# Kernel optimization log

Hardware: AMD Instinct MI355X
Metric: run time of the kernel (lower is better)

Reference implementation:

```python
import jax, jax.numpy as jnp
import numpy as np

B, N, D, K = 1024, 36, 256, 8  # batch, num_features(fixed 36 by docstring), embed_size, text_K


def setup_inputs() -> dict:
    key = jax.random.key(0)
    ks = jax.random.split(key, 5)
    texts = jax.random.normal(ks[0], (B, N, D), dtype=jnp.float32)
    # Xavier-uniform-style init matching module.init_weights()
    r_k = np.sqrt(6.0) / np.sqrt(D + D)
    r_v = np.sqrt(6.0) / np.sqrt(D + K)
    r_u = np.sqrt(6.0) / np.sqrt(K + 1)
    W = jax.random.uniform(ks[1], (K, D, D), minval=-r_k, maxval=r_k, dtype=jnp.float32)
    Wb = jnp.zeros((K, D), dtype=jnp.float32)
    V1w = jax.random.uniform(ks[2], (K, D), minval=-r_v, maxval=r_v, dtype=jnp.float32)
    V1b = jnp.zeros((K,), dtype=jnp.float32)
    V2w = jax.random.uniform(ks[3], (K, D), minval=-r_v, maxval=r_v, dtype=jnp.float32)
    V2b = jnp.zeros((K,), dtype=jnp.float32)
    Uw = jax.random.uniform(ks[4], (K,), minval=-r_u, maxval=r_u, dtype=jnp.float32)
    Ub = jnp.zeros((), dtype=jnp.float32)
    return {"texts": texts, "W": W, "Wb": Wb, "V1w": V1w, "V1b": V1b,
            "V2w": V2w, "V2b": V2b, "Uw": Uw, "Ub": Ub}


def reference(texts, W, Wb, V1w, V1b, V2w, V2b, Uw, Ub):
    # bilinear term: (W_k x_n + b_k) . x_m  -> [B,K,N,N]
    Wx = jnp.einsum('kcd,bnd->bknc', W, texts) + Wb[None, :, None, :]
    first = jnp.einsum('bknc,bmc->bknm', Wx, texts)
    # outer-sum term: V1.x_n + V2.x_m (per k)
    v1 = jnp.einsum('kd,bnd->bkn', V1w, texts) + V1b[None, :, None]  # [B,K,N]
    v2 = jnp.einsum('kd,bmd->bkm', V2w, texts) + V2b[None, :, None]  # [B,K,N]
    T = jnp.tanh(first + v1[..., None] + v2[:, :, None, :])  # [B,K,N,N]
    # faithful to torch: flatten [K,N,N] contiguously then view as (N*N, K)
    flat = T.reshape(T.shape[0], N * N, K)
    logits = (flat @ Uw + Ub).reshape(T.shape[0], N, N)
    return jax.nn.softmax(logits, axis=-1)
```

## Files before the change

kernel.cpp:

```cpp
#include <hip/hip_runtime.h>
#include <math.h>

#define NB 1024
#define NF 36
#define ED 256
#define NK 8
#define NN2 1296
#define QPK 162

typedef _Float16 f16;
typedef f16 f16x4 __attribute__((ext_vector_type(4)));
typedef f16 f16x8 __attribute__((ext_vector_type(8)));
typedef float f32x4 __attribute__((ext_vector_type(4)));

#define WXSTR 136
#define WXHSZ 13056
#define NFRAG 1536

#define XH_OFF  0
#define WXH_OFF 24576
#define V_OFF   (24576 + WXHSZ)
#define SMEM_MAIN (V_OFF + (72 + 72 + 9 + 324) * 4)

#define PVH_OFF 0
#define PVL_OFF 8192
#define PP_OFF  16384
#define SMEM_PREP 28672

#define TWO_LOG2E 2.8853900817779268f
#define C1F (0.0625f * TWO_LOG2E)

__device__ __forceinline__ f32x4 mfma16(f16x8 a, f16x8 b, f32x4 c) {
    return __builtin_amdgcn_mfma_f32_16x16x32_f16(a, b, c, 0, 0, 0);
}

__global__ __launch_bounds__(256, 4) void prep_all(
    const float* __restrict__ W, f16x8* __restrict__ WfH,
    const float* __restrict__ texts, f16x8* __restrict__ XfH,
    const float* __restrict__ V1w, const float* __restrict__ V1b,
    const float* __restrict__ V2w, const float* __restrict__ V2b,
    const float* __restrict__ Wb, float* __restrict__ v12)
{
    extern __shared__ char psmem[];
    const int blk = blockIdx.x;
    const int t = threadIdx.x;
    const int wave = t >> 6, lane = t & 63;

    if (blk < 128) {
        const int k = blk >> 4, ct = blk & 15;
        f16* Wl = (f16*)psmem;
        {
            const int r = t >> 4, seg = t & 15;
            const float* src = W + ((size_t)(k * 256 + ct * 16 + r)) * 256 + seg * 16;
            f16* d = Wl + r * 264 + seg * 16;
            #pragma unroll
            for (int j4 = 0; j4 < 4; ++j4) {
                float4 a = ((const float4*)src)[j4];
                d[j4 * 4 + 0] = (f16)(a.x * 16.0f);
                d[j4 * 4 + 1] = (f16)(a.y * 16.0f);
                d[j4 * 4 + 2] = (f16)(a.z * 16.0f);
                d[j4 * 4 + 3] = (f16)(a.w * 16.0f);
            }
        }
        __syncthreads();
        f16x8* dst = WfH + (size_t)(k * 16 + ct) * 8 * 64;
        #pragma unroll
        for (int e0 = 0; e0 < 2; ++e0) {
            const int e = t + e0 * 256;
            const int kc = e >> 6, el = e & 63, qd = el >> 4, l15 = el & 15;
            dst[e] = *(const f16x8*)(Wl + l15 * 264 + (kc * 4 + qd) * 8);
        }
        return;
    }

    f16x8* VfH = (f16x8*)(psmem + PVH_OFF);
    f16x8* VfL = (f16x8*)(psmem + PVL_OFF);
    f32x4* Pp  = (f32x4*)(psmem + PP_OFF);

    const int b = blk - 128;
    const float* xb = texts + (size_t)b * NF * ED;

    #pragma unroll
    for (int i0 = 0; i0 < 2; ++i0) {
        int i = t + i0 * 256;
        int kc = (i >> 6) & 7, ln = i & 63;
        int q = ln >> 4, col = ln & 15;
        int which = col >> 3, kk = col & 7;
        const float* src  = (which ? V2w : V1w) + kk * 256 + kc * 32 + q * 8;
        const float* srcb = Wb + kk * 256 + kc * 32 + q * 8;
        f16x8 hi, lo;
        #pragma unroll
        for (int j = 0; j < 8; ++j) {
            float sv = src[j] + (which ? srcb[j] : 0.f);
            sv *= 16.0f;
            f16 h = (f16)sv;
            hi[j] = h;
            lo[j] = (f16)(sv - (float)h);
        }
        VfH[i] = hi;
        VfL[i] = lo;
    }

    f16x8 FH[6], FL[6];
    #pragma unroll
    for (int i0 = 0; i0 < 6; ++i0) {
        int i = t + i0 * 256;
        int rt = i >> 9, kc = (i >> 6) & 7;
        int q = lane >> 4, l15 = lane & 15;
        int row = rt * 16 + l15;
        f16x8 hi, lo;
        if (row < NF) {
            const float* s = xb + row * ED + kc * 32 + q * 8;
            float4 a = *(const float4*)s;
            float4 c = *(const float4*)(s + 4);
            float v[8] = {a.x, a.y, a.z, a.w, c.x, c.y, c.z, c.w};
            #pragma unroll
            for (int j = 0; j < 8; ++j) {
                f16 h = (f16)v[j];
                hi[j] = h;
                lo[j] = (f16)(v[j] - (float)h);
            }
        } else {
            #pragma unroll
            for (int j = 0; j < 8; ++j) { hi[j] = (f16)0.f; lo[j] = (f16)0.f; }
        }
        FH[i0] = hi;
        FL[i0] = lo;
        XfH[(size_t)b * NFRAG + i] = hi;
    }
    __syncthreads();

    f32x4 pacc[3];
    #pragma unroll
    for (int rt = 0; rt < 3; ++rt) pacc[rt] = (f32x4){0.f, 0.f, 0.f, 0.f};
    #pragma unroll
    for (int rt = 0; rt < 3; ++rt) {
        #pragma unroll
        for (int s = 0; s < 2; ++s) {
            const int i0 = rt * 2 + s;
            const int kc = wave + 4 * s;
            f16x8 bh = VfH[kc * 64 + lane];
            f16x8 bl = VfL[kc * 64 + lane];
            pacc[rt] = mfma16(FH[i0], bh, pacc[rt]);
            pacc[rt] = mfma16(FH[i0], bl, pacc[rt]);
            pacc[rt] = mfma16(FL[i0], bh, pacc[rt]);
        }
    }
    #pragma unroll
    for (int rt = 0; rt < 3; ++rt)
        Pp[(wave * 3 + rt) * 64 + lane] = pacc[rt];
    __syncthreads();

    if (wave < 3) {
        f32x4 acc = Pp[(0 * 3 + wave) * 64 + lane];
        #pragma unroll
        for (int w = 1; w < 4; ++w) acc += Pp[(w * 3 + wave) * 64 + lane];
        const int q = lane >> 4, l15 = lane & 15;
        const int which = l15 >> 3, kk = l15 & 7;
        const float bias = which ? V2b[kk] : V1b[kk];
        #pragma unroll
        for (int r = 0; r < 4; ++r) {
            const int n = wave * 16 + q * 4 + r;
            if (n < NF)
                v12[((size_t)b * 16 + l15) * NF + n] = acc[r] * 0.0625f + bias;
        }
    }
}

#define P1_STEP(ACC, WKP, H, KC) do {                                         \
    f16x8 w0_ = (WKP)[((((H) * 8 + wave) * 8) + (KC)) * 64 + lane];           \
    f16x8 w1_ = (WKP)[((((H) * 8 + wave + 4) * 8) + (KC)) * 64 + lane];       \
    _Pragma("unroll")                                                         \
    for (int rt_ = 0; rt_ < 3; ++rt_) {                                       \
        f16x8 ah_ = Xh[(rt_ * 8 + (KC)) * 64 + lane];                         \
        ACC[rt_][0] = mfma16(w0_, ah_, ACC[rt_][0]);                          \
        ACC[rt_][1] = mfma16(w1_, ah_, ACC[rt_][1]);                          \
    }                                                                         \
} while (0)

#define P2_TILE(IT, H, KK) do {                                               \
    const int p_ = wave + (IT) * 4;                                           \
    if (p_ < 9) {                                                             \
        const int nt_ = p_ / 3, mt_ = p_ % 3;                                 \
        const f16* wp_ = Wxh + (nt_ * 16 + l15) * WXSTR + quad * 8;           \
        _Pragma("unroll")                                                     \
        for (int kc2_ = 0; kc2_ < 4; ++kc2_) {                                \
            f16x8 pah_ = *(const f16x8*)(wp_ + kc2_ * 32);                    \
            f16x8 pbh_ = Xh[(mt_ * 8 + (H) * 4 + kc2_) * 64 + lane];          \
            sacc[KK][IT] = mfma16(pah_, pbh_, sacc[KK][IT]);                  \
        }                                                                     \
    }                                                                         \
} while (0)

#define ZERO_ACC(ACC) do {                                                    \
    _Pragma("unroll")                                                         \
    for (int i_ = 0; i_ < 3; ++i_) {                                          \
        ACC[i_][0] = (f32x4){0.f, 0.f, 0.f, 0.f};                             \
        ACC[i_][1] = (f32x4){0.f, 0.f, 0.f, 0.f};                             \
    }                                                                         \
} while (0)

#define STORE_WX(ACC) do {                                                    \
    _Pragma("unroll")                                                         \
    for (int rt_ = 0; rt_ < 3; ++rt_) {                                       \
        const int n_ = rt_ * 16 + l15;                                        \
        _Pragma("unroll")                                                     \
        for (int j2_ = 0; j2_ < 2; ++j2_) {                                   \
            const int cb_ = (j2_ ? (wave + 4) : wave) * 16 + quad * 4;        \
            f16x4 h4_;                                                        \
            _Pragma("unroll")                                                 \
            for (int r_ = 0; r_ < 4; ++r_) h4_[r_] = (f16)(ACC[rt_][j2_][r_]);\
            *(f16x4*)(Wxh + n_ * WXSTR + cb_) = h4_;                          \
        }                                                                     \
    }                                                                         \
} while (0)

#define SEG_FUSED(ACC, WKP, H1, HP, KKP) do {                                 \
    _Pragma("unroll")                                                         \
    for (int kc_ = 0; kc_ < 8; ++kc_) {                                       \
        P1_STEP(ACC, WKP, H1, kc_);                                           \
        if (kc_ == 1) P2_TILE(0, HP, KKP);                                    \
        if (kc_ == 3) P2_TILE(1, HP, KKP);                                    \
        if (kc_ == 5) P2_TILE(2, HP, KKP);                                    \
    }                                                                         \
} while (0)

__global__ __launch_bounds__(256, 4) void ntn_main(
    const f16x8* __restrict__ XfHG,
    const f16x8* __restrict__ WfH,
    const float* __restrict__ v12,
    const float* __restrict__ Uw, const float* __restrict__ Ubp,
    float* __restrict__ out)
{
    extern __shared__ char smem[];
    f16x8* Xh   = (f16x8*)(smem + XH_OFF);
    f16*   Wxh  = (f16*)(smem + WXH_OFF);
    float* v1s2 = (float*)(smem + V_OFF);
    float* v2s2 = v1s2 + 72;
    float* Uws  = v1s2 + 144;
    float* Ls   = v1s2 + 153;

    const int id  = blockIdx.x;
    const int xcd = id & 7;
    const int rem = id >> 3;
    const int kp  = rem & 3;
    const int b   = ((rem >> 2) << 3) | xcd;
    const int k0  = kp * 2;

    const int t    = threadIdx.x;
    const int wave = t >> 6;
    const int lane = t & 63;
    const int quad = lane >> 4;
    const int l15  = lane & 15;

    {
        const f16x8* gh = XfHG + (size_t)b * NFRAG;
        #pragma unroll
        for (int i = 0; i < 6; ++i) Xh[t + i * 256] = gh[t + i * 256];
    }
    if (t < 144) {
        const int r = t / 36, n = t - r * 36;
        const int which = r & 1, kq = r >> 1;
        float v = v12[((size_t)b * 16 + which * 8 + (k0 + kq)) * NF + n] * TWO_LOG2E;
        (which ? v2s2 : v1s2)[kq * 36 + n] = v;
    }
    if (t < 8) Uws[t] = Uw[t];
    if (t == 8) Uws[8] = Ubp[0];
    __syncthreads();

    const f16x8* Wk0 = WfH + (size_t)k0 * 8192;
    const f16x8* Wk1 = Wk0 + 8192;

    f32x4 sacc[2][3];
    #pragma unroll
    for (int kk = 0; kk < 2; ++kk)
        #pragma unroll
        for (int it = 0; it < 3; ++it) sacc[kk][it] = (f32x4){0.f, 0.f, 0.f, 0.f};

    f32x4 acc[3][2];

    ZERO_ACC(acc);
    #pragma unroll
    for (int kc = 0; kc < 8; ++kc) P1_STEP(acc, Wk0, 0, kc);
    STORE_WX(acc);
    __syncthreads();

    ZERO_ACC(acc);
    SEG_FUSED(acc, Wk1, 0, 0, 0);
    __syncthreads();
    STORE_WX(acc);
    __syncthreads();

    ZERO_ACC(acc);
    SEG_FUSED(acc, Wk0, 1, 0, 1);
    __syncthreads();
    STORE_WX(acc);
    __syncthreads();

    ZERO_ACC(acc);
    SEG_FUSED(acc, Wk1, 1, 1, 0);
    __syncthreads();
    STORE_WX(acc);
    __syncthreads();

    P2_TILE(0, 1, 1);
    P2_TILE(1, 1, 1);
    P2_TILE(2, 1, 1);

    __syncthreads();
    float* Ts = (float*)Wxh;
    #pragma unroll
    for (int kk = 0; kk < 2; ++kk)
        #pragma unroll
        for (int it = 0; it < 3; ++it) {
            const int p = wave + it * 4;
            if (p < 9) {
                const int nt = p / 3, mt = p % 3;
                const int m = mt * 16 + l15;
                if (m < NF) {
                    #pragma unroll
                    for (int r = 0; r < 4; ++r) {
                        const int n = nt * 16 + quad * 4 + r;
                        if (n < NF) {
                            float x = sacc[kk][it][r] * C1F
                                      + v1s2[kk * 36 + n] + v2s2[kk * 36 + m];
                            float e = exp2f(x);
                            const int idx = kk * NN2 + n * NF + m;
                            Ts[idx + (idx >> 3)] = 1.f - 2.f / (e + 1.f);
                        }
                    }
                }
            }
        }
    __syncthreads();
    #pragma unroll
    for (int u0 = 0; u0 < 2; ++u0) {
        const int u = t + u0 * 256;
        if (u < 324) {
            const float* tp = Ts + u * 9;
            float lg = Uws[8];
            #pragma unroll
            for (int j = 0; j < 8; ++j) lg += Uws[j] * tp[j];
            Ls[u] = lg;
        }
    }
    __syncthreads();
    #pragma unroll
    for (int rr0 = 0; rr0 < 3; ++rr0) {
        const int rr = wave + rr0 * 4;
        if (rr < 9) {
            float v = (lane < NF) ? Ls[rr * 36 + lane] : -INFINITY;
            float mx = v;
            #pragma unroll
            for (int off = 32; off > 0; off >>= 1) mx = fmaxf(mx, __shfl_xor(mx, off));
            float e = (lane < NF) ? __expf(v - mx) : 0.f;
            float sm = e;
            #pragma unroll
            for (int off = 32; off > 0; off >>= 1) sm += __shfl_xor(sm, off);
            if (lane < NF)
                out[(size_t)b * NN2 + kp * 324 + rr * 36 + lane] = e / sm;
        }
    }
}

extern "C" void kernel_launch(void* const* d_in, const int* in_sizes, int n_in,
                              void* d_out, int out_size, void* d_ws, size_t ws_size,
                              hipStream_t stream) {
    const float* texts = (const float*)d_in[0];
    const float* W     = (const float*)d_in[1];
    const float* Wb    = (const float*)d_in[2];
    const float* V1w   = (const float*)d_in[3];
    const float* V1b   = (const float*)d_in[4];
    const float* V2w   = (const float*)d_in[5];
    const float* V2b   = (const float*)d_in[6];
    const float* Uw    = (const float*)d_in[7];
    const float* Ub    = (const float*)d_in[8];

    char* ws = (char*)d_ws;
    f16x8* WfH = (f16x8*)ws;
    f16x8* XfH = (f16x8*)(ws + (1 << 20));
    float* v12 = (float*)(ws + (1 << 20) + (size_t)NB * NFRAG * 16);
    float* outp = (float*)d_out;

    hipFuncSetAttribute((const void*)prep_all,
                        hipFuncAttributeMaxDynamicSharedMemorySize, SMEM_PREP);
    hipFuncSetAttribute((const void*)ntn_main,
                        hipFuncAttributeMaxDynamicSharedMemorySize, SMEM_MAIN);

    prep_all<<<128 + NB, 256, SMEM_PREP, stream>>>(W, WfH, texts, XfH,
                                                   V1w, V1b, V2w, V2b, Wb, v12);
    ntn_main<<<NB * NK / 2, 256, SMEM_MAIN, stream>>>(XfH, WfH, v12, Uw, Ub, outp);
}
```

Baseline: 182.0 us.

## Process both K slices per phase with compacted padded X tile in LDS

Restructures the main kernel so each phase computes Wx for both k slices at once, sharing each X fragment load across four MFMAs and halving the number of phase/barrier rounds. The padded third row tile of X is compacted into a small LDS region, with a shared zero buffer serving the padding rows, and Wx rows beyond 36 are neither stored nor read. LDS is reorganized into two Wx buffers. This doubles accumulator registers (acc becomes 3x2x2), which may pressure occupancy at the 4-blocks launch bound.

```diff
diff --git a/kernel.cpp b/kernel.cpp
--- a/kernel.cpp
+++ b/kernel.cpp
@@ -6,7 +6,6 @@
 #define ED 256
 #define NK 8
 #define NN2 1296
-#define QPK 162
 
 typedef _Float16 f16;
 typedef f16 f16x4 __attribute__((ext_vector_type(4)));
@@ -14,12 +13,13 @@
 typedef float f32x4 __attribute__((ext_vector_type(4)));
 
 #define WXSTR 136
-#define WXHSZ 13056
 #define NFRAG 1536
 
-#define XH_OFF  0
-#define WXH_OFF 24576
-#define V_OFF   (24576 + WXHSZ)
+#define XC2_OFF 16384
+#define ZB_OFF  18432
+#define WX0_OFF 18448
+#define WX1_OFF (WX0_OFF + 9792)
+#define V_OFF   (WX1_OFF + 9792)
 #define SMEM_MAIN (V_OFF + (72 + 72 + 9 + 324) * 4)
 
 #define PVH_OFF 0
@@ -32,6 +32,15 @@
 
 __device__ __forceinline__ f32x4 mfma16(f16x8 a, f16x8 b, f32x4 c) {
     return __builtin_amdgcn_mfma_f32_16x16x32_f16(a, b, c, 0, 0, 0);
+}
+
+__device__ __forceinline__ const f16x8* xfragp(const char* smem, int f, int lane) {
+    const int l15 = lane & 15, q = (lane >> 4) & 3;
+    int off;
+    if (f < 16) off = (f * 64 + lane) * 16;
+    else        off = (l15 < 4) ? (XC2_OFF + (((f - 16) * 16) + q * 4 + l15) * 16)
+                                : ZB_OFF;
+    return (const f16x8*)(smem + off);
 }
 
 __global__ __launch_bounds__(256, 4) void prep_all(
@@ -167,61 +176,68 @@
     }
 }
 
-#define P1_STEP(ACC, WKP, H, KC) do {                                         \
-    f16x8 w0_ = (WKP)[((((H) * 8 + wave) * 8) + (KC)) * 64 + lane];           \
-    f16x8 w1_ = (WKP)[((((H) * 8 + wave + 4) * 8) + (KC)) * 64 + lane];       \
+#define P1S(ACC, H, KC) do {                                                  \
+    f16x8 w00_ = Wk0[((((H) * 8 + wave) * 8) + (KC)) * 64 + lane];            \
+    f16x8 w01_ = Wk0[((((H) * 8 + wave + 4) * 8) + (KC)) * 64 + lane];        \
+    f16x8 w10_ = Wk1[((((H) * 8 + wave) * 8) + (KC)) * 64 + lane];            \
+    f16x8 w11_ = Wk1[((((H) * 8 + wave + 4) * 8) + (KC)) * 64 + lane];        \
     _Pragma("unroll")                                                         \
     for (int rt_ = 0; rt_ < 3; ++rt_) {                                       \
-        f16x8 ah_ = Xh[(rt_ * 8 + (KC)) * 64 + lane];                         \
-        ACC[rt_][0] = mfma16(w0_, ah_, ACC[rt_][0]);                          \
-        ACC[rt_][1] = mfma16(w1_, ah_, ACC[rt_][1]);                          \
+        f16x8 ah_ = *xfragp(smem, rt_ * 8 + (KC), lane);                      \
+        ACC[rt_][0][0] = mfma16(w00_, ah_, ACC[rt_][0][0]);                   \
+        ACC[rt_][1][0] = mfma16(w01_, ah_, ACC[rt_][1][0]);                   \
+        ACC[rt_][0][1] = mfma16(w10_, ah_, ACC[rt_][0][1]);                   \
+        ACC[rt_][1][1] = mfma16(w11_, ah_, ACC[rt_][1][1]);                   \
     }                                                                         \
 } while (0)
 
-#define P2_TILE(IT, H, KK) do {                                               \
+#define P2_TILE2(IT, H) do {                                                  \
     const int p_ = wave + (IT) * 4;                                           \
     if (p_ < 9) {                                                             \
         const int nt_ = p_ / 3, mt_ = p_ % 3;                                 \
-        const f16* wp_ = Wxh + (nt_ * 16 + l15) * WXSTR + quad * 8;           \
+        const int row_ = nt_ * 16 + l15;                                      \
+        const int cr_ = row_ > 35 ? 35 : row_;    \
+        const f16* w0p_ = Wxh0 + cr_ * WXSTR + quad * 8;                      \
+        const f16* w1p_ = Wxh1 + cr_ * WXSTR + quad * 8;                      \
         _Pragma("unroll")                                                     \
         for (int kc2_ = 0; kc2_ < 4; ++kc2_) {                                \
-            f16x8 pah_ = *(const f16x8*)(wp_ + kc2_ * 32);                    \
-            f16x8 pbh_ = Xh[(mt_ * 8 + (H) * 4 + kc2_) * 64 + lane];          \
-            sacc[KK][IT] = mfma16(pah_, pbh_, sacc[KK][IT]);                  \
+            f16x8 xb_ = *xfragp(smem, mt_ * 8 + (H) * 4 + kc2_, lane);        \
+            f16x8 a0_ = *(const f16x8*)(w0p_ + kc2_ * 32);                    \
+            f16x8 a1_ = *(const f16x8*)(w1p_ + kc2_ * 32);                    \
+            sacc[0][IT] = mfma16(a0_, xb_, sacc[0][IT]);                      \
+            sacc[1][IT] = mfma16(a1_, xb_, sacc[1][IT]);                      \
         }                                                                     \
     }                                                                         \
 } while (0)
 
 #define ZERO_ACC(ACC) do {                                                    \
     _Pragma("unroll")                                                         \
-    for (int i_ = 0; i_ < 3; ++i_) {                                          \
-        ACC[i_][0] = (f32x4){0.f, 0.f, 0.f, 0.f};                             \
-        ACC[i_][1] = (f32x4){0.f, 0.f, 0.f, 0.f};                             \
-    }                                                                         \
+    for (int i_ = 0; i_ < 3; ++i_)                                            \
+        _Pragma("unroll")                                                     \
+        for (int j_ = 0; j_ < 2; ++j_) {                                      \
+            ACC[i_][j_][0] = (f32x4){0.f, 0.f, 0.f, 0.f};                     \
+            ACC[i_][j_][1] = (f32x4){0.f, 0.f, 0.f, 0.f};                     \
+        }                                                                     \
 } while (0)
 
-#define STORE_WX(ACC) do {                                                    \
+#define STORE_WX2(ACC) do {                                                   \
     _Pragma("unroll")                                                         \
     for (int rt_ = 0; rt_ < 3; ++rt_) {                                       \
         const int n_ = rt_ * 16 + l15;                                        \
-        _Pragma("unroll")                                                     \
-        for (int j2_ = 0; j2_ < 2; ++j2_) {                                   \
-            const int cb_ = (j2_ ? (wave + 4) : wave) * 16 + quad * 4;        \
-            f16x4 h4_;                                                        \
+        if (rt_ < 2 || l15 < 4) {                                             \
             _Pragma("unroll")                                                 \
-            for (int r_ = 0; r_ < 4; ++r_) h4_[r_] = (f16)(ACC[rt_][j2_][r_]);\
-            *(f16x4*)(Wxh + n_ * WXSTR + cb_) = h4_;                          \
+            for (int j2_ = 0; j2_ < 2; ++j2_) {                               \
+                const int cb_ = (j2_ ? (wave + 4) : wave) * 16 + quad * 4;    \
+                f16x4 h0_, h1_;                                               \
+                _Pragma("unroll")                                             \
+                for (int r_ = 0; r_ < 4; ++r_) {                              \
+                    h0_[r_] = (f16)(ACC[rt_][j2_][0][r_]);                    \
+                    h1_[r_] = (f16)(ACC[rt_][j2_][1][r_]);                    \
+                }                                                             \
+                *(f16x4*)(Wxh0 + n_ * WXSTR + cb_) = h0_;                     \
+                *(f16x4*)(Wxh1 + n_ * WXSTR + cb_) = h1_;                     \
+            }                                                                 \
         }                                                                     \
-    }                                                                         \
-} while (0)
-
-#define SEG_FUSED(ACC, WKP, H1, HP, KKP) do {                                 \
-    _Pragma("unroll")                                                         \
-    for (int kc_ = 0; kc_ < 8; ++kc_) {                                       \
-        P1_STEP(ACC, WKP, H1, kc_);                                           \
-        if (kc_ == 1) P2_TILE(0, HP, KKP);                                    \
-        if (kc_ == 3) P2_TILE(1, HP, KKP);                                    \
-        if (kc_ == 5) P2_TILE(2, HP, KKP);                                    \
     }                                                                         \
 } while (0)
 
@@ -233,8 +249,8 @@
     float* __restrict__ out)
 {
     extern __shared__ char smem[];
-    f16x8* Xh   = (f16x8*)(smem + XH_OFF);
-    f16*   Wxh  = (f16*)(smem + WXH_OFF);
+    f16*   Wxh0 = (f16*)(smem + WX0_OFF);
+    f16*   Wxh1 = (f16*)(smem + WX1_OFF);
     float* v1s2 = (float*)(smem + V_OFF);
     float* v2s2 = v1s2 + 72;
     float* Uws  = v1s2 + 144;
@@ -256,7 +272,22 @@
     {
         const f16x8* gh = XfHG + (size_t)b * NFRAG;
         #pragma unroll
-        for (int i = 0; i < 6; ++i) Xh[t + i * 256] = gh[t + i * 256];
+        for (int i0 = 0; i0 < 4; ++i0)
+            *(f16x8*)(smem + (size_t)(t + i0 * 256) * 16) = gh[t + i0 * 256];
+        #pragma unroll
+        for (int i0 = 4; i0 < 6; ++i0) {
+            const int e = t + i0 * 256;
+            f16x8 v = gh[e];
+            const int kc = (e >> 6) - 16;
+            if (l15 < 4)
+                *(f16x8*)(smem + XC2_OFF + (size_t)(kc * 16 + quad * 4 + l15) * 16) = v;
+        }
+        if (t == 0) {
+            f16x8 z;
+            #pragma unroll
+            for (int j = 0; j < 8; ++j) z[j] = (f16)0.f;
+            *(f16x8*)(smem + ZB_OFF) = z;
+        }
     }
     if (t < 144) {
         const int r = t / 36, n = t - r * 36;
@@ -277,38 +308,32 @@
         #pragma unroll
         for (int it = 0; it < 3; ++it) sacc[kk][it] = (f32x4){0.f, 0.f, 0.f, 0.f};
 
-    f32x4 acc[3][2];
+    f32x4 acc[3][2][2];
 
     ZERO_ACC(acc);
     #pragma unroll
-    for (int kc = 0; kc < 8; ++kc) P1_STEP(acc, Wk0, 0, kc);
-    STORE_WX(acc);
+    for (int kc = 0; kc < 8; ++kc) P1S(acc, 0, kc);
+    STORE_WX2(acc);
     __syncthreads();
 
     ZERO_ACC(acc);
-    SEG_FUSED(acc, Wk1, 0, 0, 0);
-    __syncthreads();
-    STORE_WX(acc);
-    __syncthreads();
-
-    ZERO_ACC(acc);
-    SEG_FUSED(acc, Wk0, 1, 0, 1);
-    __syncthreads();
-    STORE_WX(acc);
-    __syncthreads();
-
-    ZERO_ACC(acc);
-    SEG_FUSED(acc, Wk1, 1, 1, 0);
-    __syncthreads();
-    STORE_WX(acc);
-    __syncthreads();
-
-    P2_TILE(0, 1, 1);
-    P2_TILE(1, 1, 1);
-    P2_TILE(2, 1, 1);
-
-    __syncthreads();
-    float* Ts = (float*)Wxh;
+    #pragma unroll
+    for (int kc = 0; kc < 8; ++kc) {
+        P1S(acc, 1, kc);
+        if (kc == 1) P2_TILE2(0, 0);
+        if (kc == 3) P2_TILE2(1, 0);
+        if (kc == 5) P2_TILE2(2, 0);
+    }
+    __syncthreads();
+    STORE_WX2(acc);
+    __syncthreads();
+
+    P2_TILE2(0, 1);
+    P2_TILE2(1, 1);
+    P2_TILE2(2, 1);
+
+    __syncthreads();
+    float* Ts = (float*)Wxh0;
     #pragma unroll
     for (int kk = 0; kk < 2; ++kk)
         #pragma unroll
```

Measured after the change: 190.5 us. +4.7%, slower.

## Fuse per-batch text conversion and V projection into main kernel

Applied to the files above, without the earlier changes.

Moves the fp32-to-fp16 hi/lo conversion of texts and the V1/V2 projection out of the prep kernel and into ntn_main. Each main block now reads raw texts, builds its X fragments in LDS, and computes the v1/v2 terms itself, reusing the Wx LDS area as reduction scratch. This drops the XfH and v12 workspace round trip and shrinks the prep kernel to W packing only. In exchange, the per-batch conversion and projection MFMAs are repeated in each of the four blocks per batch, and an extra barrier is added before the first Wx store.

```diff
diff --git a/kernel.cpp b/kernel.cpp
--- a/kernel.cpp
+++ b/kernel.cpp
@@ -6,7 +6,6 @@
 #define ED 256
 #define NK 8
 #define NN2 1296
-#define QPK 162
 
 typedef _Float16 f16;
 typedef f16 f16x4 __attribute__((ext_vector_type(4)));
@@ -22,10 +21,7 @@
 #define V_OFF   (24576 + WXHSZ)
 #define SMEM_MAIN (V_OFF + (72 + 72 + 9 + 324) * 4)
 
-#define PVH_OFF 0
-#define PVL_OFF 8192
-#define PP_OFF  16384
-#define SMEM_PREP 28672
+#define SMEM_PREP 8448
 
 #define TWO_LOG2E 2.8853900817779268f
 #define C1F (0.0625f * TWO_LOG2E)
@@ -34,136 +30,34 @@
     return __builtin_amdgcn_mfma_f32_16x16x32_f16(a, b, c, 0, 0, 0);
 }
 
-__global__ __launch_bounds__(256, 4) void prep_all(
-    const float* __restrict__ W, f16x8* __restrict__ WfH,
-    const float* __restrict__ texts, f16x8* __restrict__ XfH,
-    const float* __restrict__ V1w, const float* __restrict__ V1b,
-    const float* __restrict__ V2w, const float* __restrict__ V2b,
-    const float* __restrict__ Wb, float* __restrict__ v12)
+__global__ __launch_bounds__(256, 4) void wpack(
+    const float* __restrict__ W, f16x8* __restrict__ WfH)
 {
     extern __shared__ char psmem[];
     const int blk = blockIdx.x;
     const int t = threadIdx.x;
-    const int wave = t >> 6, lane = t & 63;
-
-    if (blk < 128) {
-        const int k = blk >> 4, ct = blk & 15;
-        f16* Wl = (f16*)psmem;
-        {
-            const int r = t >> 4, seg = t & 15;
-            const float* src = W + ((size_t)(k * 256 + ct * 16 + r)) * 256 + seg * 16;
-            f16* d = Wl + r * 264 + seg * 16;
-            #pragma unroll
-            for (int j4 = 0; j4 < 4; ++j4) {
-                float4 a = ((const float4*)src)[j4];
-                d[j4 * 4 + 0] = (f16)(a.x * 16.0f);
-                d[j4 * 4 + 1] = (f16)(a.y * 16.0f);
-                d[j4 * 4 + 2] = (f16)(a.z * 16.0f);
-                d[j4 * 4 + 3] = (f16)(a.w * 16.0f);
-            }
-        }
-        __syncthreads();
-        f16x8* dst = WfH + (size_t)(k * 16 + ct) * 8 * 64;
-        #pragma unroll
-        for (int e0 = 0; e0 < 2; ++e0) {
-            const int e = t + e0 * 256;
-            const int kc = e >> 6, el = e & 63, qd = el >> 4, l15 = el & 15;
-            dst[e] = *(const f16x8*)(Wl + l15 * 264 + (kc * 4 + qd) * 8);
-        }
-        return;
-    }
-
-    f16x8* VfH = (f16x8*)(psmem + PVH_OFF);
-    f16x8* VfL = (f16x8*)(psmem + PVL_OFF);
-    f32x4* Pp  = (f32x4*)(psmem + PP_OFF);
-
-    const int b = blk - 128;
-    const float* xb = texts + (size_t)b * NF * ED;
-
-    #pragma unroll
-    for (int i0 = 0; i0 < 2; ++i0) {
-        int i = t + i0 * 256;
-        int kc = (i >> 6) & 7, ln = i & 63;
-        int q = ln >> 4, col = ln & 15;
-        int which = col >> 3, kk = col & 7;
-        const float* src  = (which ? V2w : V1w) + kk * 256 + kc * 32 + q * 8;
-        const float* srcb = Wb + kk * 256 + kc * 32 + q * 8;
-        f16x8 hi, lo;
-        #pragma unroll
-        for (int j = 0; j < 8; ++j) {
-            float sv = src[j] + (which ? srcb[j] : 0.f);
-            sv *= 16.0f;
-            f16 h = (f16)sv;
-            hi[j] = h;
-            lo[j] = (f16)(sv - (float)h);
-        }
-        VfH[i] = hi;
-        VfL[i] = lo;
-    }
-
-    f16x8 FH[6], FL[6];
-    #pragma unroll
-    for (int i0 = 0; i0 < 6; ++i0) {
-        int i = t + i0 * 256;
-        int rt = i >> 9, kc = (i >> 6) & 7;
-        int q = lane >> 4, l15 = lane & 15;
-        int row = rt * 16 + l15;
-        f16x8 hi, lo;
-        if (row < NF) {
-            const float* s = xb + row * ED + kc * 32 + q * 8;
-            float4 a = *(const float4*)s;
-            float4 c = *(const float4*)(s + 4);
-            float v[8] = {a.x, a.y, a.z, a.w, c.x, c.y, c.z, c.w};
-            #pragma unroll
-            for (int j = 0; j < 8; ++j) {
-                f16 h = (f16)v[j];
-                hi[j] = h;
-                lo[j] = (f16)(v[j] - (float)h);
-            }
-        } else {
-            #pragma unroll
-            for (int j = 0; j < 8; ++j) { hi[j] = (f16)0.f; lo[j] = (f16)0.f; }
-        }
-        FH[i0] = hi;
-        FL[i0] = lo;
-        XfH[(size_t)b * NFRAG + i] = hi;
-    }
-    __syncthreads();
-
-    f32x4 pacc[3];
-    #pragma unroll
-    for (int rt = 0; rt < 3; ++rt) pacc[rt] = (f32x4){0.f, 0.f, 0.f, 0.f};
-    #pragma unroll
-    for (int rt = 0; rt < 3; ++rt) {
-        #pragma unroll
-        for (int s = 0; s < 2; ++s) {
-            const int i0 = rt * 2 + s;
-            const int kc = wave + 4 * s;
-            f16x8 bh = VfH[kc * 64 + lane];
-            f16x8 bl = VfL[kc * 64 + lane];
-            pacc[rt] = mfma16(FH[i0], bh, pacc[rt]);
-            pacc[rt] = mfma16(FH[i0], bl, pacc[rt]);
-            pacc[rt] = mfma16(FL[i0], bh, pacc[rt]);
-        }
-    }
-    #pragma unroll
-    for (int rt = 0; rt < 3; ++rt)
-        Pp[(wave * 3 + rt) * 64 + lane] = pacc[rt];
-    __syncthreads();
-
-    if (wave < 3) {
-        f32x4 acc = Pp[(0 * 3 + wave) * 64 + lane];
-        #pragma unroll
-        for (int w = 1; w < 4; ++w) acc += Pp[(w * 3 + wave) * 64 + lane];
-        const int q = lane >> 4, l15 = lane & 15;
-        const int which = l15 >> 3, kk = l15 & 7;
-        const float bias = which ? V2b[kk] : V1b[kk];
-        #pragma unroll
-        for (int r = 0; r < 4; ++r) {
-            const int n = wave * 16 + q * 4 + r;
-            if (n < NF)
-                v12[((size_t)b * 16 + l15) * NF + n] = acc[r] * 0.0625f + bias;
-        }
+    const int k = blk >> 4, ct = blk & 15;
+    f16* Wl = (f16*)psmem;
+    {
+        const int r = t >> 4, seg = t & 15;
+        const float* src = W + ((size_t)(k * 256 + ct * 16 + r)) * 256 + seg * 16;
+        f16* d = Wl + r * 264 + seg * 16;
+        #pragma unroll
+        for (int j4 = 0; j4 < 4; ++j4) {
+            float4 a = ((const float4*)src)[j4];
+            d[j4 * 4 + 0] = (f16)(a.x * 16.0f);
+            d[j4 * 4 + 1] = (f16)(a.y * 16.0f);
+            d[j4 * 4 + 2] = (f16)(a.z * 16.0f);
+            d[j4 * 4 + 3] = (f16)(a.w * 16.0f);
+        }
+    }
+    __syncthreads();
+    f16x8* dst = WfH + (size_t)(k * 16 + ct) * 8 * 64;
+    #pragma unroll
+    for (int e0 = 0; e0 < 2; ++e0) {
+        const int e = t + e0 * 256;
+        const int kc = e >> 6, el = e & 63, qd = el >> 4, l15 = el & 15;
+        dst[e] = *(const f16x8*)(Wl + l15 * 264 + (kc * 4 + qd) * 8);
     }
 }
 
@@ -226,9 +120,11 @@
 } while (0)
 
 __global__ __launch_bounds__(256, 4) void ntn_main(
-    const f16x8* __restrict__ XfHG,
+    const float* __restrict__ texts,
     const f16x8* __restrict__ WfH,
-    const float* __restrict__ v12,
+    const float* __restrict__ V1w, const float* __restrict__ V1b,
+    const float* __restrict__ V2w, const float* __restrict__ V2b,
+    const float* __restrict__ Wb,
     const float* __restrict__ Uw, const float* __restrict__ Ubp,
     float* __restrict__ out)
 {
@@ -253,21 +149,90 @@
     const int quad = lane >> 4;
     const int l15  = lane & 15;
 
+    const float* xb = texts + (size_t)b * NF * ED;
+    f16x8 FH[6], FL[6];
+    #pragma unroll
+    for (int i0 = 0; i0 < 6; ++i0) {
+        const int i = t + i0 * 256;
+        const int rt = i >> 9, kc = (i >> 6) & 7;
+        const int row = rt * 16 + l15;
+        f16x8 hi, lo;
+        if (row < NF) {
+            const float* s = xb + row * ED + kc * 32 + quad * 8;
+            float4 a = *(const float4*)s;
+            float4 c = *(const float4*)(s + 4);
+            float v[8] = {a.x, a.y, a.z, a.w, c.x, c.y, c.z, c.w};
+            #pragma unroll
+            for (int j = 0; j < 8; ++j) {
+                f16 h = (f16)v[j];
+                hi[j] = h;
+                lo[j] = (f16)(v[j] - (float)h);
+            }
+        } else {
+            #pragma unroll
+            for (int j = 0; j < 8; ++j) { hi[j] = (f16)0.f; lo[j] = (f16)0.f; }
+        }
+        FH[i0] = hi;
+        FL[i0] = lo;
+        Xh[i] = hi;
+    }
+    f16x8 VH[2], VL[2];
+    #pragma unroll
+    for (int s = 0; s < 2; ++s) {
+        const int kcv = wave + 4 * s;
+        const int which = l15 >> 3, kk = l15 & 7;
+        const float* src  = (which ? V2w : V1w) + kk * 256 + kcv * 32 + quad * 8;
+        const float* srcb = Wb + kk * 256 + kcv * 32 + quad * 8;
+        #pragma unroll
+        for (int j = 0; j < 8; ++j) {
+            float sv = src[j] + (which ? srcb[j] : 0.f);
+            sv *= 16.0f;
+            f16 h = (f16)sv;
+            VH[s][j] = h;
+            VL[s][j] = (f16)(sv - (float)h);
+        }
+    }
     {
-        const f16x8* gh = XfHG + (size_t)b * NFRAG;
-        #pragma unroll
-        for (int i = 0; i < 6; ++i) Xh[t + i * 256] = gh[t + i * 256];
-    }
-    if (t < 144) {
-        const int r = t / 36, n = t - r * 36;
-        const int which = r & 1, kq = r >> 1;
-        float v = v12[((size_t)b * 16 + which * 8 + (k0 + kq)) * NF + n] * TWO_LOG2E;
-        (which ? v2s2 : v1s2)[kq * 36 + n] = v;
+        f32x4 pacc[3];
+        #pragma unroll
+        for (int rt = 0; rt < 3; ++rt) pacc[rt] = (f32x4){0.f, 0.f, 0.f, 0.f};
+        #pragma unroll
+        for (int rt = 0; rt < 3; ++rt)
+            #pragma unroll
+            for (int s = 0; s < 2; ++s) {
+                const int i0 = rt * 2 + s;
+                pacc[rt] = mfma16(FH[i0], VH[s], pacc[rt]);
+                pacc[rt] = mfma16(FH[i0], VL[s], pacc[rt]);
+                pacc[rt] = mfma16(FL[i0], VH[s], pacc[rt]);
+            }
+        f32x4* Pp = (f32x4*)Wxh;
+        #pragma unroll
+        for (int rt = 0; rt < 3; ++rt)
+            Pp[(wave * 3 + rt) * 64 + lane] = pacc[rt];
     }
     if (t < 8) Uws[t] = Uw[t];
     if (t == 8) Uws[8] = Ubp[0];
     __syncthreads();
 
+    if (wave < 3) {
+        const f32x4* Pp = (const f32x4*)Wxh;
+        f32x4 racc = Pp[(0 * 3 + wave) * 64 + lane];
+        #pragma unroll
+        for (int w = 1; w < 4; ++w) racc += Pp[(w * 3 + wave) * 64 + lane];
+        const int which = l15 >> 3, kk = l15 & 7;
+        if (kk == k0 || kk == k0 + 1) {
+            const int kidx = kk - k0;
+            const float bias = which ? V2b[kk] : V1b[kk];
+            #pragma unroll
+            for (int r = 0; r < 4; ++r) {
+                const int n = wave * 16 + quad * 4 + r;
+                if (n < NF)
+                    (which ? v2s2 : v1s2)[kidx * 36 + n] =
+                        (racc[r] * 0.0625f + bias) * TWO_LOG2E;
+            }
+        }
+    }
+
     const f16x8* Wk0 = WfH + (size_t)k0 * 8192;
     const f16x8* Wk1 = Wk0 + 8192;
 
@@ -282,6 +247,7 @@
     ZERO_ACC(acc);
     #pragma unroll
     for (int kc = 0; kc < 8; ++kc) P1_STEP(acc, Wk0, 0, kc);
+    __syncthreads();
     STORE_WX(acc);
     __syncthreads();
 
@@ -378,16 +344,15 @@
 
     char* ws = (char*)d_ws;
     f16x8* WfH = (f16x8*)ws;
-    f16x8* XfH = (f16x8*)(ws + (1 << 20));
-    float* v12 = (float*)(ws + (1 << 20) + (size_t)NB * NFRAG * 16);
     float* outp = (float*)d_out;
 
-    hipFuncSetAttribute((const void*)prep_all,
+    hipFuncSetAttribute((const void*)wpack,
                         hipFuncAttributeMaxDynamicSharedMemorySize, SMEM_PREP);
     hipFuncSetAttribute((const void*)ntn_main,
                         hipFuncAttributeMaxDynamicSharedMemorySize, SMEM_MAIN);
 
-    prep_all<<<128 + NB, 256, SMEM_PREP, stream>>>(W, WfH, texts, XfH,
-                                                   V1w, V1b, V2w, V2b, Wb, v12);
-    ntn_main<<<NB * NK / 2, 256, SMEM_MAIN, stream>>>(XfH, WfH, v12, Uw, Ub, outp);
+    wpack<<<128, 256, SMEM_PREP, stream>>>(W, WfH);
+    ntn_main<<<NB * NK / 2, 256, SMEM_MAIN, stream>>>(texts, WfH,
+                                                      V1w, V1b, V2w, V2b, Wb,
+                                                      Uw, Ub, outp);
 }
```

After: 206.4 us. 13.4% more time.
